# Optimization experiments

Measured on AMD Instinct MI355X. Metric: run time of the kernel, lower is better.

The kernel has to match this reference:

```python
import jax, jax.numpy as jnp
import numpy as np

N, D, H = 1024, 128, 512
EPS = 1e-5  # torch LayerNorm default


def setup_inputs() -> dict:
    key = jax.random.key(0)
    ks = jax.random.split(key, 8)
    emb = jax.random.normal(ks[0], (N, D), dtype=jnp.float32)
    emb = emb / jnp.linalg.norm(emb, axis=-1, keepdims=True)  # L2-normalised GAT embeddings
    s1 = 1.0 / np.sqrt(2 * D)
    s2 = 1.0 / np.sqrt(H)
    s3 = 1.0 / np.sqrt(H // 2)
    return {
        "embeddings": emb,
        "W1": jax.random.uniform(ks[1], (2 * D, H), jnp.float32, -s1, s1),
        "b1": jnp.zeros((H,), jnp.float32),
        "gamma": jnp.ones((H,), jnp.float32),
        "beta": jnp.zeros((H,), jnp.float32),
        "W2": jax.random.uniform(ks[2], (H, H // 2), jnp.float32, -s2, s2),
        "b2": jnp.zeros((H // 2,), jnp.float32),
        "W3": jax.random.uniform(ks[3], (H // 2, 1), jnp.float32, -s3, s3),
        "b3": jnp.zeros((1,), jnp.float32),
    }


def reference(embeddings, W1, b1, gamma, beta, W2, b2, W3, b3):
    n = embeddings.shape[0]
    idx_i, idx_j = jnp.triu_indices(n, k=1)          # E = n(n-1)/2
    pairs = jnp.stack([idx_i, idx_j], axis=1)        # [E, 2]
    e_i = embeddings[idx_i]                          # [E, D]
    e_j = embeddings[idx_j]
    feats = jnp.concatenate([e_i - e_j, e_i * e_j], axis=-1)  # [E, 2D]
    h = jax.nn.relu(feats @ W1 + b1)                 # [E, H]
    mu = jnp.mean(h, axis=-1, keepdims=True)
    var = jnp.mean(jnp.square(h - mu), axis=-1, keepdims=True)
    h = (h - mu) * jax.lax.rsqrt(var + EPS) * gamma + beta
    # dropout is identity at inference
    h = jax.nn.relu(h @ W2 + b2)                     # [E, H//2]
    logits = (h @ W3 + b3)[:, 0]                     # [E]
    return logits, pairs
```

## Files before the change

kernel.cpp:

```cpp
#include <hip/hip_runtime.h>

typedef __attribute__((ext_vector_type(8))) int i32x8;
typedef __attribute__((ext_vector_type(16))) float f32x16;
typedef unsigned int u32;
typedef unsigned char u8;

#define NN 1024
#define ETOT 523776
#define EPSV 1e-5f

#define L_PSUM 0
#define L_PSQ  3072
#define L_B1   6144
#define L_G    8192
#define L_BB   9216
#define L_W3   10240
#define L_TILE 11264
#define L_TOTAL 44032

#define SCL1 0x7F7F7F7F

__device__ __forceinline__ u32 pk4fp8(float a, float b, float c, float d) {
  int p = __builtin_amdgcn_cvt_pk_fp8_f32(a, b, 0, false);
  p = __builtin_amdgcn_cvt_pk_fp8_f32(c, d, p, true);
  return (u32)p;
}

struct u4x2 { uint4 a, b; };
struct u2x4 { uint2 a, b, c, d; };
__device__ __forceinline__ i32x8 ldg32(const u8* p) {
  u4x2 t; t.a = *(const uint4*)p; t.b = *(const uint4*)(p + 16);
  return __builtin_bit_cast(i32x8, t);
}
__device__ __forceinline__ i32x8 lds32(const char* base, int e8) {
  u2x4 t;
  t.a = *(const uint2*)(base + e8);
  t.b = *(const uint2*)(base + 512 + e8);
  t.c = *(const uint2*)(base + 1024 + e8);
  t.d = *(const uint2*)(base + 1536 + e8);
  return __builtin_bit_cast(i32x8, t);
}
#define MFMA64(A,B,C) __builtin_amdgcn_mfma_scale_f32_32x32x64_f8f6f4((A),(B),(C),0,0,0,SCL1,0,SCL1)

__global__ void prep_w(const float* __restrict__ W1, const float* __restrict__ W2,
                       const float* __restrict__ gammav,
                       u8* __restrict__ W1f, u8* __restrict__ W2f) {
  int idx = blockIdx.x*256 + threadIdx.x;
  { int c = idx >> 8, k = idx & 255;
    float v = W1[k*512 + c] * 64.f;
    int p = __builtin_amdgcn_cvt_pk_fp8_f32(v, 0.f, 0, false);
    W1f[(c>>5)*8192 + (k>>6)*2048 + ((k>>5)&1)*1024 + (c&31)*32 + (k&31)] = (u8)(p & 0xff); }
  { int o = idx >> 9, c = idx & 511;
    float v = gammav[c] * W2[c*256 + o] * 64.f;
    int p = __builtin_amdgcn_cvt_pk_fp8_f32(v, 0.f, 0, false);
    W2f[(o>>5)*16384 + (c>>6)*2048 + ((c>>5)&1)*1024 + (o&31)*32 + (c&31)] = (u8)(p & 0xff); }
}

__global__ void prep_vec(const float* __restrict__ W2, const float* __restrict__ gammav,
                         const float* __restrict__ betav, const float* __restrict__ b2v,
                         float* __restrict__ Gv, float* __restrict__ BBv) {
  int o = blockIdx.x, t = threadIdx.x;
  float g = 0.f, bb = 0.f;
  for (int c = t; c < 512; c += 64) {
    float w = W2[c*256 + o];
    g  += gammav[c] * w;
    bb += betav[c]  * w;
  }
  #pragma unroll
  for (int off = 1; off < 64; off <<= 1) {
    g  += __shfl_xor(g,  off, 64);
    bb += __shfl_xor(bb, off, 64);
  }
  if (t == 0) { Gv[o] = g; BBv[o] = bb + b2v[o]; }
}

__launch_bounds__(512, 4)
__global__ void edge_main(const float* __restrict__ emb,
                          const float* __restrict__ b1v,
                          const float* __restrict__ b3v,
                          const float* __restrict__ w3v,
                          const float* __restrict__ Gv,
                          const float* __restrict__ BBv,
                          const u8* __restrict__ W1f,
                          const u8* __restrict__ W2f,
                          float* __restrict__ out) {
  extern __shared__ char smem[];
  float* psum = (float*)(smem + L_PSUM);
  float* psq  = (float*)(smem + L_PSQ);
  float* sb1  = (float*)(smem + L_B1);
  float* sG   = (float*)(smem + L_G);
  float* sBB  = (float*)(smem + L_BB);
  float* sw3  = (float*)(smem + L_W3);
  char*  tile = smem + L_TILE;
  char*  A1   = tile + 16384;

  const int tid  = threadIdx.x;
  const int w    = tid >> 6;
  const int lane = tid & 63;
  const int l31  = lane & 31;
  const int hi   = lane >> 5;

  int kblk = blockIdx.x;
  int bi = (int)((257.0f - sqrtf(66049.0f - 8.0f*(float)kblk)) * 0.5f);
  bi = bi < 0 ? 0 : (bi > 127 ? 127 : bi);
  while (bi*128 - bi*(bi-1)/2 > kblk) --bi;
  while ((bi+1)*128 - (bi+1)*bi/2 <= kblk) ++bi;
  const int bj = bi + (kblk - (bi*128 - bi*(bi-1)/2));
  const int i0 = bi*8, j0 = bj*8;

  {
    const int e  = lane;
    const int d0 = (w & 3) * 32;
    const float4* pei = (const float4*)(emb + (i0 + (e>>3))*128 + d0);
    const float4* pej = (const float4*)(emb + (j0 + (e&7))*128 + d0);
    char* base = A1 + (w>>1)*4096 + (w&1)*2048 + e*8;
    #pragma unroll
    for (int s = 0; s < 4; ++s) {
      float4 x0 = pei[s*2], x1 = pei[s*2+1];
      float4 y0 = pej[s*2], y1 = pej[s*2+1];
      uint2 pk;
      if (w < 4) {
        pk.x = pk4fp8((x0.x-y0.x)*4.f, (x0.y-y0.y)*4.f, (x0.z-y0.z)*4.f, (x0.w-y0.w)*4.f);
        pk.y = pk4fp8((x1.x-y1.x)*4.f, (x1.y-y1.y)*4.f, (x1.z-y1.z)*4.f, (x1.w-y1.w)*4.f);
      } else {
        pk.x = pk4fp8((x0.x*y0.x)*4.f, (x0.y*y0.y)*4.f, (x0.z*y0.z)*4.f, (x0.w*y0.w)*4.f);
        pk.y = pk4fp8((x1.x*y1.x)*4.f, (x1.y*y1.y)*4.f, (x1.z*y1.z)*4.f, (x1.w*y1.w)*4.f);
      }
      *(uint2*)(base + s*512) = pk;
    }
  }
  sb1[tid] = b1v[tid] * 16.f;
  if (tid < 256) { sG[tid] = Gv[tid]; sBB[tid] = BBv[tid]; sw3[tid] = w3v[tid]; }
  __syncthreads();

  f32x16 z16;
  #pragma unroll
  for (int i = 0; i < 16; ++i) z16[i] = 0.f;

  float sumS0 = 0.f, sqS0 = 0.f, sumS1 = 0.f, sqS1 = 0.f;
  f32x16 A0, A1acc;

  auto h1pass = [&](int cb, const f32x16& E0, const f32x16& E1) {
    char* dbase = tile + (cb>>1)*4096 + (cb&1)*2048 + hi*4;
    #pragma unroll
    for (int g = 0; g < 4; ++g) {
      const int c0 = cb*32 + g*8 + hi*4;
      const float b0 = sb1[c0+0], b1_ = sb1[c0+1], b2_ = sb1[c0+2], b3_ = sb1[c0+3];
      char* dst = dbase + g*512;
      {
        float v0 = fmaxf(fmaf(E0[g*4+0], 0.0625f, b0), 0.f);
        float v1 = fmaxf(fmaf(E0[g*4+1], 0.0625f, b1_), 0.f);
        float v2 = fmaxf(fmaf(E0[g*4+2], 0.0625f, b2_), 0.f);
        float v3 = fmaxf(fmaf(E0[g*4+3], 0.0625f, b3_), 0.f);
        *(u32*)(dst + l31*8) = pk4fp8(v0, v1, v2, v3);
        sumS0 += (v0+v1)+(v2+v3);
        sqS0 = fmaf(v0,v0,sqS0); sqS0 = fmaf(v1,v1,sqS0);
        sqS0 = fmaf(v2,v2,sqS0); sqS0 = fmaf(v3,v3,sqS0);
      }
      {
        float v0 = fmaxf(fmaf(E1[g*4+0], 0.0625f, b0), 0.f);
        float v1 = fmaxf(fmaf(E1[g*4+1], 0.0625f, b1_), 0.f);
        float v2 = fmaxf(fmaf(E1[g*4+2], 0.0625f, b2_), 0.f);
        float v3 = fmaxf(fmaf(E1[g*4+3], 0.0625f, b3_), 0.f);
        *(u32*)(dst + (l31+32)*8) = pk4fp8(v0, v1, v2, v3);
        sumS1 += (v0+v1)+(v2+v3);
        sqS1 = fmaf(v0,v0,sqS1); sqS1 = fmaf(v1,v1,sqS1);
        sqS1 = fmaf(v2,v2,sqS1); sqS1 = fmaf(v3,v3,sqS1);
      }
    }
  };

  const u8* w1base = W1f + hi*1024 + l31*32;

  A0 = z16; A1acc = z16;
  __builtin_amdgcn_s_setprio(1);
  #pragma unroll
  for (int kq = 0; kq < 4; ++kq) {
    i32x8 af = ldg32(w1base + w*8192 + kq*2048);
    const char* bbp = A1 + kq*4096 + hi*2048;
    i32x8 bf0 = lds32(bbp, l31*8);
    i32x8 bf1 = lds32(bbp, (l31+32)*8);
    A0    = MFMA64(af, bf0, A0);
    A1acc = MFMA64(af, bf1, A1acc);
  }
  __builtin_amdgcn_s_setprio(0);
  h1pass(w, A0, A1acc);

  A0 = z16; A1acc = z16;
  __builtin_amdgcn_s_setprio(1);
  #pragma unroll
  for (int kq = 0; kq < 4; ++kq) {
    i32x8 af = ldg32(w1base + (w+8)*8192 + kq*2048);
    const char* bbp = A1 + kq*4096 + hi*2048;
    i32x8 bf0 = lds32(bbp, l31*8);
    i32x8 bf1 = lds32(bbp, (l31+32)*8);
    A0    = MFMA64(af, bf0, A0);
    A1acc = MFMA64(af, bf1, A1acc);
  }
  __builtin_amdgcn_s_setprio(0);
  __syncthreads();
  h1pass(w + 8, A0, A1acc);

  sumS0 += __shfl_xor(sumS0, 32, 64);  sqS0 += __shfl_xor(sqS0, 32, 64);
  sumS1 += __shfl_xor(sumS1, 32, 64);  sqS1 += __shfl_xor(sqS1, 32, 64);
  if (hi == 0) {
    psum[l31*12 + w] = sumS0;       psq[l31*12 + w] = sqS0;
    psum[(l31+32)*12 + w] = sumS1;  psq[(l31+32)*12 + w] = sqS1;
  }
  __syncthreads();

  float sc2A, smA, sc2B, smB;
  {
    float4 s0 = *(const float4*)(psum + l31*12);
    float4 s1 = *(const float4*)(psum + l31*12 + 4);
    float4 q0 = *(const float4*)(psq  + l31*12);
    float4 q1 = *(const float4*)(psq  + l31*12 + 4);
    float su = ((s0.x+s0.y)+(s0.z+s0.w)) + ((s1.x+s1.y)+(s1.z+s1.w));
    float qu = ((q0.x+q0.y)+(q0.z+q0.w)) + ((q1.x+q1.y)+(q1.z+q1.w));
    float mu = su * (1.f/8192.f);
    float sc = rsqrtf(qu * (1.f/131072.f) - mu*mu + EPSV);
    sc2A = sc * (1.f/1024.f); smA = mu * sc;
    s0 = *(const float4*)(psum + (l31+32)*12);
    s1 = *(const float4*)(psum + (l31+32)*12 + 4);
    q0 = *(const float4*)(psq  + (l31+32)*12);
    q1 = *(const float4*)(psq  + (l31+32)*12 + 4);
    su = ((s0.x+s0.y)+(s0.z+s0.w)) + ((s1.x+s1.y)+(s1.z+s1.w));
    qu = ((q0.x+q0.y)+(q0.z+q0.w)) + ((q1.x+q1.y)+(q1.z+q1.w));
    mu = su * (1.f/8192.f);
    sc = rsqrtf(qu * (1.f/131072.f) - mu*mu + EPSV);
    sc2B = sc * (1.f/1024.f); smB = mu * sc;
  }

  f32x16 C0 = z16, C1 = z16;
  {
    const u8* w2base = W2f + w*16384 + hi*1024 + l31*32;
    __builtin_amdgcn_s_setprio(1);
    #pragma unroll
    for (int kq = 0; kq < 8; ++kq) {
      i32x8 a = ldg32(w2base + kq*2048);
      const char* bbp = tile + kq*4096 + hi*2048;
      i32x8 b0 = lds32(bbp, l31*8);
      i32x8 b1 = lds32(bbp, (l31+32)*8);
      C0 = MFMA64(a, b0, C0);
      C1 = MFMA64(a, b1, C1);
    }
    __builtin_amdgcn_s_setprio(0);
  }

  {
    float p0 = 0.f, p1 = 0.f;
    #pragma unroll
    for (int rg = 0; rg < 16; ++rg) {
      const int o = w*32 + (rg&3) + 8*(rg>>2) + 4*hi;
      const float gv = sG[o], bb = sBB[o], w3 = sw3[o];
      float t0 = fmaxf(fmaf(sc2A, C0[rg], fmaf(-smA, gv, bb)), 0.f);
      p0 = fmaf(t0, w3, p0);
      float t1 = fmaxf(fmaf(sc2B, C1[rg], fmaf(-smB, gv, bb)), 0.f);
      p1 = fmaf(t1, w3, p1);
    }
    p0 += __shfl_xor(p0, 32, 64);
    p1 += __shfl_xor(p1, 32, 64);
    if (hi == 0) {
      sb1[l31*8 + w] = p0;
      sb1[(l31+32)*8 + w] = p1;
    }
  }
  __syncthreads();

  if (tid < 64) {
    float4 s0 = *(const float4*)(sb1 + tid*8);
    float4 s1 = *(const float4*)(sb1 + tid*8 + 4);
    float logit = ((s0.x+s0.y)+(s0.z+s0.w)) + ((s1.x+s1.y)+(s1.z+s1.w)) + b3v[0];
    int a = tid >> 3, b = tid & 7;
    int i = i0 + a, j = j0 + b;
    if (i < j) {
      int e = i*(2*NN - i - 1)/2 + (j - i - 1);
      out[e] = logit;
      out[ETOT + 2*e]     = (float)i;
      out[ETOT + 2*e + 1] = (float)j;
    }
  }
}

extern "C" void kernel_launch(void* const* d_in, const int* in_sizes, int n_in,
                              void* d_out, int out_size, void* d_ws, size_t ws_size,
                              hipStream_t stream) {
  const float* emb   = (const float*)d_in[0];
  const float* W1    = (const float*)d_in[1];
  const float* b1    = (const float*)d_in[2];
  const float* gamma = (const float*)d_in[3];
  const float* beta  = (const float*)d_in[4];
  const float* W2    = (const float*)d_in[5];
  const float* b2    = (const float*)d_in[6];
  const float* W3    = (const float*)d_in[7];
  const float* b3    = (const float*)d_in[8];

  char* ws   = (char*)d_ws;
  u8*  W1f = (u8*)ws;
  u8*  W2f = (u8*)(ws + 131072);
  float* Gv  = (float*)(ws + 262144);
  float* BBv = (float*)(ws + 263168);

  (void)hipFuncSetAttribute((const void*)edge_main,
                            hipFuncAttributeMaxDynamicSharedMemorySize, L_TOTAL);

  prep_w<<<512, 256, 0, stream>>>(W1, W2, gamma, W1f, W2f);
  prep_vec<<<256, 64, 0, stream>>>(W2, gamma, beta, b2, Gv, BBv);
  edge_main<<<8256, 512, L_TOTAL, stream>>>(emb, b1, b3, W3, Gv, BBv,
                                            W1f, W2f, (float*)d_out);
}
```

Before: 210.4 us.

## Separate layer-1 input buffer from hidden tile and drop mid-kernel barrier

The fp8 pair-feature buffer gets its own shared-memory region instead of aliasing the hidden-activation tile, which lets the __syncthreads between the two layer-1 passes go. Several smaller changes ride along. The x4 feature scaling moves into a prescaled embedding copy plus a per-K-block MFMA scale for the difference half, G/BB/W3 are packed into one float4 table, bias loads are vectorised, and the s_setprio hints are removed. Shared memory per block grows from about 44 KB to 61 KB, which can lower how many blocks fit on a CU.

```diff
diff --git a/kernel.cpp b/kernel.cpp
--- a/kernel.cpp
+++ b/kernel.cpp
@@ -12,13 +12,13 @@
 #define L_PSUM 0
 #define L_PSQ  3072
 #define L_B1   6144
-#define L_G    8192
-#define L_BB   9216
-#define L_W3   10240
-#define L_TILE 11264
-#define L_TOTAL 44032
+#define L_GBW  8192
+#define L_TILE 12288
+#define L_A1   45056
+#define L_TOTAL 61440
 
 #define SCL1 0x7F7F7F7F
+#define SCL2 0x80808080
 
 __device__ __forceinline__ u32 pk4fp8(float a, float b, float c, float d) {
   int p = __builtin_amdgcn_cvt_pk_fp8_f32(a, b, 0, false);
@@ -40,11 +40,13 @@
   t.d = *(const uint2*)(base + 1536 + e8);
   return __builtin_bit_cast(i32x8, t);
 }
-#define MFMA64(A,B,C) __builtin_amdgcn_mfma_scale_f32_32x32x64_f8f6f4((A),(B),(C),0,0,0,SCL1,0,SCL1)
+__device__ __forceinline__ f32x16 mfma64(i32x8 A, i32x8 B, f32x16 C, int sB) {
+  return __builtin_amdgcn_mfma_scale_f32_32x32x64_f8f6f4(A, B, C, 0, 0, 0, SCL1, 0, sB);
+}
 
 __global__ void prep_w(const float* __restrict__ W1, const float* __restrict__ W2,
-                       const float* __restrict__ gammav,
-                       u8* __restrict__ W1f, u8* __restrict__ W2f) {
+                       const float* __restrict__ gammav, const float* __restrict__ emb,
+                       u8* __restrict__ W1f, u8* __restrict__ W2f, float* __restrict__ emb2) {
   int idx = blockIdx.x*256 + threadIdx.x;
   { int c = idx >> 8, k = idx & 255;
     float v = W1[k*512 + c] * 64.f;
@@ -54,11 +56,12 @@
     float v = gammav[c] * W2[c*256 + o] * 64.f;
     int p = __builtin_amdgcn_cvt_pk_fp8_f32(v, 0.f, 0, false);
     W2f[(o>>5)*16384 + (c>>6)*2048 + ((c>>5)&1)*1024 + (o&31)*32 + (c&31)] = (u8)(p & 0xff); }
+  emb2[idx] = emb[idx] * 2.f;
 }
 
 __global__ void prep_vec(const float* __restrict__ W2, const float* __restrict__ gammav,
                          const float* __restrict__ betav, const float* __restrict__ b2v,
-                         float* __restrict__ Gv, float* __restrict__ BBv) {
+                         const float* __restrict__ w3v, float4* __restrict__ GBWv) {
   int o = blockIdx.x, t = threadIdx.x;
   float g = 0.f, bb = 0.f;
   for (int c = t; c < 512; c += 64) {
@@ -71,16 +74,14 @@
     g  += __shfl_xor(g,  off, 64);
     bb += __shfl_xor(bb, off, 64);
   }
-  if (t == 0) { Gv[o] = g; BBv[o] = bb + b2v[o]; }
+  if (t == 0) GBWv[o] = make_float4(g, bb + b2v[o], w3v[o], 0.f);
 }
 
 __launch_bounds__(512, 4)
-__global__ void edge_main(const float* __restrict__ emb,
+__global__ void edge_main(const float* __restrict__ emb2,
                           const float* __restrict__ b1v,
                           const float* __restrict__ b3v,
-                          const float* __restrict__ w3v,
-                          const float* __restrict__ Gv,
-                          const float* __restrict__ BBv,
+                          const float4* __restrict__ GBWv,
                           const u8* __restrict__ W1f,
                           const u8* __restrict__ W2f,
                           float* __restrict__ out) {
@@ -88,11 +89,9 @@
   float* psum = (float*)(smem + L_PSUM);
   float* psq  = (float*)(smem + L_PSQ);
   float* sb1  = (float*)(smem + L_B1);
-  float* sG   = (float*)(smem + L_G);
-  float* sBB  = (float*)(smem + L_BB);
-  float* sw3  = (float*)(smem + L_W3);
+  float4* sgbw= (float4*)(smem + L_GBW);
   char*  tile = smem + L_TILE;
-  char*  A1   = tile + 16384;
+  char*  A1   = smem + L_A1;
 
   const int tid  = threadIdx.x;
   const int w    = tid >> 6;
@@ -111,8 +110,8 @@
   {
     const int e  = lane;
     const int d0 = (w & 3) * 32;
-    const float4* pei = (const float4*)(emb + (i0 + (e>>3))*128 + d0);
-    const float4* pej = (const float4*)(emb + (j0 + (e&7))*128 + d0);
+    const float4* pei = (const float4*)(emb2 + (i0 + (e>>3))*128 + d0);
+    const float4* pej = (const float4*)(emb2 + (j0 + (e&7))*128 + d0);
     char* base = A1 + (w>>1)*4096 + (w&1)*2048 + e*8;
     #pragma unroll
     for (int s = 0; s < 4; ++s) {
@@ -120,17 +119,17 @@
       float4 y0 = pej[s*2], y1 = pej[s*2+1];
       uint2 pk;
       if (w < 4) {
-        pk.x = pk4fp8((x0.x-y0.x)*4.f, (x0.y-y0.y)*4.f, (x0.z-y0.z)*4.f, (x0.w-y0.w)*4.f);
-        pk.y = pk4fp8((x1.x-y1.x)*4.f, (x1.y-y1.y)*4.f, (x1.z-y1.z)*4.f, (x1.w-y1.w)*4.f);
+        pk.x = pk4fp8(x0.x-y0.x, x0.y-y0.y, x0.z-y0.z, x0.w-y0.w);
+        pk.y = pk4fp8(x1.x-y1.x, x1.y-y1.y, x1.z-y1.z, x1.w-y1.w);
       } else {
-        pk.x = pk4fp8((x0.x*y0.x)*4.f, (x0.y*y0.y)*4.f, (x0.z*y0.z)*4.f, (x0.w*y0.w)*4.f);
-        pk.y = pk4fp8((x1.x*y1.x)*4.f, (x1.y*y1.y)*4.f, (x1.z*y1.z)*4.f, (x1.w*y1.w)*4.f);
+        pk.x = pk4fp8(x0.x*y0.x, x0.y*y0.y, x0.z*y0.z, x0.w*y0.w);
+        pk.y = pk4fp8(x1.x*y1.x, x1.y*y1.y, x1.z*y1.z, x1.w*y1.w);
       }
       *(uint2*)(base + s*512) = pk;
     }
   }
   sb1[tid] = b1v[tid] * 16.f;
-  if (tid < 256) { sG[tid] = Gv[tid]; sBB[tid] = BBv[tid]; sw3[tid] = w3v[tid]; }
+  if (tid < 256) sgbw[tid] = GBWv[tid];
   __syncthreads();
 
   f32x16 z16;
@@ -145,23 +144,23 @@
     #pragma unroll
     for (int g = 0; g < 4; ++g) {
       const int c0 = cb*32 + g*8 + hi*4;
-      const float b0 = sb1[c0+0], b1_ = sb1[c0+1], b2_ = sb1[c0+2], b3_ = sb1[c0+3];
+      const float4 b4 = *(const float4*)(sb1 + c0);
       char* dst = dbase + g*512;
       {
-        float v0 = fmaxf(fmaf(E0[g*4+0], 0.0625f, b0), 0.f);
-        float v1 = fmaxf(fmaf(E0[g*4+1], 0.0625f, b1_), 0.f);
-        float v2 = fmaxf(fmaf(E0[g*4+2], 0.0625f, b2_), 0.f);
-        float v3 = fmaxf(fmaf(E0[g*4+3], 0.0625f, b3_), 0.f);
+        float v0 = fmaxf(fmaf(E0[g*4+0], 0.0625f, b4.x), 0.f);
+        float v1 = fmaxf(fmaf(E0[g*4+1], 0.0625f, b4.y), 0.f);
+        float v2 = fmaxf(fmaf(E0[g*4+2], 0.0625f, b4.z), 0.f);
+        float v3 = fmaxf(fmaf(E0[g*4+3], 0.0625f, b4.w), 0.f);
         *(u32*)(dst + l31*8) = pk4fp8(v0, v1, v2, v3);
         sumS0 += (v0+v1)+(v2+v3);
         sqS0 = fmaf(v0,v0,sqS0); sqS0 = fmaf(v1,v1,sqS0);
         sqS0 = fmaf(v2,v2,sqS0); sqS0 = fmaf(v3,v3,sqS0);
       }
       {
-        float v0 = fmaxf(fmaf(E1[g*4+0], 0.0625f, b0), 0.f);
-        float v1 = fmaxf(fmaf(E1[g*4+1], 0.0625f, b1_), 0.f);
-        float v2 = fmaxf(fmaf(E1[g*4+2], 0.0625f, b2_), 0.f);
-        float v3 = fmaxf(fmaf(E1[g*4+3], 0.0625f, b3_), 0.f);
+        float v0 = fmaxf(fmaf(E1[g*4+0], 0.0625f, b4.x), 0.f);
+        float v1 = fmaxf(fmaf(E1[g*4+1], 0.0625f, b4.y), 0.f);
+        float v2 = fmaxf(fmaf(E1[g*4+2], 0.0625f, b4.z), 0.f);
+        float v3 = fmaxf(fmaf(E1[g*4+3], 0.0625f, b4.w), 0.f);
         *(u32*)(dst + (l31+32)*8) = pk4fp8(v0, v1, v2, v3);
         sumS1 += (v0+v1)+(v2+v3);
         sqS1 = fmaf(v0,v0,sqS1); sqS1 = fmaf(v1,v1,sqS1);
@@ -173,32 +172,29 @@
   const u8* w1base = W1f + hi*1024 + l31*32;
 
   A0 = z16; A1acc = z16;
-  __builtin_amdgcn_s_setprio(1);
   #pragma unroll
   for (int kq = 0; kq < 4; ++kq) {
+    const int sB = (kq < 2) ? SCL2 : SCL1;
     i32x8 af = ldg32(w1base + w*8192 + kq*2048);
     const char* bbp = A1 + kq*4096 + hi*2048;
     i32x8 bf0 = lds32(bbp, l31*8);
     i32x8 bf1 = lds32(bbp, (l31+32)*8);
-    A0    = MFMA64(af, bf0, A0);
-    A1acc = MFMA64(af, bf1, A1acc);
-  }
-  __builtin_amdgcn_s_setprio(0);
+    A0    = mfma64(af, bf0, A0, sB);
+    A1acc = mfma64(af, bf1, A1acc, sB);
+  }
   h1pass(w, A0, A1acc);
 
   A0 = z16; A1acc = z16;
-  __builtin_amdgcn_s_setprio(1);
   #pragma unroll
   for (int kq = 0; kq < 4; ++kq) {
+    const int sB = (kq < 2) ? SCL2 : SCL1;
     i32x8 af = ldg32(w1base + (w+8)*8192 + kq*2048);
     const char* bbp = A1 + kq*4096 + hi*2048;
     i32x8 bf0 = lds32(bbp, l31*8);
     i32x8 bf1 = lds32(bbp, (l31+32)*8);
-    A0    = MFMA64(af, bf0, A0);
-    A1acc = MFMA64(af, bf1, A1acc);
-  }
-  __builtin_amdgcn_s_setprio(0);
-  __syncthreads();
+    A0    = mfma64(af, bf0, A0, sB);
+    A1acc = mfma64(af, bf1, A1acc, sB);
+  }
   h1pass(w + 8, A0, A1acc);
 
   sumS0 += __shfl_xor(sumS0, 32, 64);  sqS0 += __shfl_xor(sqS0, 32, 64);
@@ -234,17 +230,15 @@
   f32x16 C0 = z16, C1 = z16;
   {
     const u8* w2base = W2f + w*16384 + hi*1024 + l31*32;
-    __builtin_amdgcn_s_setprio(1);
     #pragma unroll
     for (int kq = 0; kq < 8; ++kq) {
       i32x8 a = ldg32(w2base + kq*2048);
       const char* bbp = tile + kq*4096 + hi*2048;
       i32x8 b0 = lds32(bbp, l31*8);
       i32x8 b1 = lds32(bbp, (l31+32)*8);
-      C0 = MFMA64(a, b0, C0);
-      C1 = MFMA64(a, b1, C1);
-    }
-    __builtin_amdgcn_s_setprio(0);
+      C0 = mfma64(a, b0, C0, SCL1);
+      C1 = mfma64(a, b1, C1, SCL1);
+    }
   }
 
   {
@@ -252,11 +246,11 @@
     #pragma unroll
     for (int rg = 0; rg < 16; ++rg) {
       const int o = w*32 + (rg&3) + 8*(rg>>2) + 4*hi;
-      const float gv = sG[o], bb = sBB[o], w3 = sw3[o];
-      float t0 = fmaxf(fmaf(sc2A, C0[rg], fmaf(-smA, gv, bb)), 0.f);
-      p0 = fmaf(t0, w3, p0);
-      float t1 = fmaxf(fmaf(sc2B, C1[rg], fmaf(-smB, gv, bb)), 0.f);
-      p1 = fmaf(t1, w3, p1);
+      const float4 t = sgbw[o];
+      float t0 = fmaxf(fmaf(sc2A, C0[rg], fmaf(-smA, t.x, t.y)), 0.f);
+      p0 = fmaf(t0, t.z, p0);
+      float t1 = fmaxf(fmaf(sc2B, C1[rg], fmaf(-smB, t.x, t.y)), 0.f);
+      p1 = fmaf(t1, t.z, p1);
     }
     p0 += __shfl_xor(p0, 32, 64);
     p1 += __shfl_xor(p1, 32, 64);
@@ -298,14 +292,14 @@
   char* ws   = (char*)d_ws;
   u8*  W1f = (u8*)ws;
   u8*  W2f = (u8*)(ws + 131072);
-  float* Gv  = (float*)(ws + 262144);
-  float* BBv = (float*)(ws + 263168);
+  float4* GBWv = (float4*)(ws + 262144);
+  float* emb2  = (float*)(ws + 266240);
 
   (void)hipFuncSetAttribute((const void*)edge_main,
                             hipFuncAttributeMaxDynamicSharedMemorySize, L_TOTAL);
 
-  prep_w<<<512, 256, 0, stream>>>(W1, W2, gamma, W1f, W2f);
-  prep_vec<<<256, 64, 0, stream>>>(W2, gamma, beta, b2, Gv, BBv);
-  edge_main<<<8256, 512, L_TOTAL, stream>>>(emb, b1, b3, W3, Gv, BBv,
+  prep_w<<<512, 256, 0, stream>>>(W1, W2, gamma, emb, W1f, W2f, emb2);
+  prep_vec<<<256, 64, 0, stream>>>(W2, gamma, beta, b2, W3, GBWv);
+  edge_main<<<8256, 512, L_TOTAL, stream>>>(emb2, b1, b3, GBWv,
                                             W1f, W2f, (float*)d_out);
 }
```

Measured after the change: 370.3 us. +76.0%, slower.
